# Kernel optimization log

Measured on AMD Instinct MI355X. Metric: run time of the kernel, lower is better.

The kernel has to match this reference:

```python
import jax, jax.numpy as jnp
import numpy as np

B, N, H, HID, LOCALITY = 2, 4096, 4, 256, 30.0
VD = HID // H
F32_MAX = jnp.finfo(jnp.float32).max


def setup_inputs() -> dict:
    key = jax.random.key(0)
    k1, k2, k3, k4 = jax.random.split(key, 4)
    m_dist = jax.random.uniform(k1, (B, N, N), dtype=jnp.float32)  # pairwise distances (b,N,N)
    x = jax.random.normal(k2, (B, N, HID), dtype=jnp.float32)
    r = jax.random.normal(k3, (1, H, 1, 1), dtype=jnp.float32)  # learned per-head distance scale
    # lecun_normal: std = 1/sqrt(fan_in), fan_in = HID
    weight = jax.random.normal(k4, (H, HID, VD), dtype=jnp.float32) / np.sqrt(HID)
    return {"m_dist": m_dist, "x": x, "r": r, "weight": weight}


def reference(m_dist, x, r, weight):
    # scaled distance per head: (b,h,n,n)
    scaled = m_dist[:, None, :, :] * (r ** 2)
    # percentile-thresholded local mask (linear interpolation, per row)
    thresh = jnp.percentile(scaled, LOCALITY, axis=-1, keepdims=True, method="linear")
    scaled = jnp.where(scaled <= thresh, scaled, F32_MAX)
    att = jax.nn.softmax(-scaled, axis=-1)  # (b,h,n,n)
    value = jnp.einsum("bnj,hjk->bhnk", x, weight)  # (b,h,n,v)
    out = jnp.einsum("bhnj,bhjd->bhnd", att, value)  # (b,h,n,v)
    out = jnp.transpose(out, (0, 2, 1, 3)).reshape(out.shape[0], -1, HID)  # (b,n,hid)
    return jax.nn.gelu(out, approximate=False)
```

## Files before the change

### kernel.cpp

```cpp
#include <hip/hip_runtime.h>
#include <hip/hip_bf16.h>

#define Bc   2
#define Nc   4096
#define Hc   4
#define HIDc 256
#define VDc  64

typedef short s8v  __attribute__((ext_vector_type(8)));
typedef float f4v  __attribute__((ext_vector_type(4)));

static __device__ __forceinline__ unsigned short bf16bits(float f) {
    __hip_bfloat16 h = __float2bfloat16(f);
    return *(unsigned short*)&h;
}

__global__ __launch_bounds__(256) void front_kernel(
    const float* __restrict__ m_dist, const float* __restrict__ wgt,
    unsigned short* __restrict__ wh, unsigned short* __restrict__ wl,
    float* __restrict__ thr_out, float* __restrict__ min_out)
{
    int t = threadIdx.x, bid = blockIdx.x;

    if (bid < 128) {
        int h  = bid >> 5;
        int kt = (bid >> 3) & 3;
        int jc = bid & 7;
        int lane = t >> 2, ii = t & 3;
        #pragma unroll
        for (int u = 0; u < 2; u++) {
            int i = ii * 2 + u;
            int j = jc * 32 + (lane >> 4) * 8 + i;
            int k = kt * 16 + (lane & 15);
            float v = wgt[((size_t)h * HIDc + j) * VDc + k];
            __hip_bfloat16 hb = __float2bfloat16(v);
            float hf = __bfloat162float(hb);
            size_t o = ((((size_t)h * 4 + kt) * 8 + jc) * 64 + lane) * 8 + i;
            wh[o] = *(unsigned short*)&hb;
            wl[o] = bf16bits(v - hf);
        }
        return;
    }

    __shared__ unsigned int hist[1024];
    __shared__ float wredf[4];
    __shared__ unsigned int wsum[4];
    __shared__ unsigned int wscan[4];
    __shared__ int b0s, b1s;
    __shared__ unsigned int c0s;
    __shared__ unsigned int ncand;
    __shared__ float cand[256];
    __shared__ float s0s, s1s;

    size_t rowid = bid - 128;
    const float* row = m_dist + rowid * Nc;

    float4 vals[4];
    float lmin = 1e30f;
    #pragma unroll
    for (int i = 0; i < 4; i++) {
        float4 v = ((const float4*)row)[t + i * 256];
        vals[i] = v;
        lmin = fminf(lmin, fminf(fminf(v.x, v.y), fminf(v.z, v.w)));
    }
    #pragma unroll
    for (int o = 32; o > 0; o >>= 1) lmin = fminf(lmin, __shfl_xor(lmin, o));
    if ((t & 63) == 0) wredf[t >> 6] = lmin;

    const unsigned int R0 = 1228u, R1 = 1229u;
    float wlo = 0.25f, whi = 0.35f;
    int b0 = 0, b1 = 0;
    unsigned int C0 = 0;

    for (;;) {
        float wscale = 1024.0f / (whi - wlo);

        for (int i = t; i < 1024; i += 256) hist[i] = 0u;
        if (t == 0) ncand = 0u;
        __syncthreads();

        unsigned int cb = 0;
        #pragma unroll
        for (int i = 0; i < 4; i++) {
            float a[4] = {vals[i].x, vals[i].y, vals[i].z, vals[i].w};
            #pragma unroll
            for (int j = 0; j < 4; j++) {
                float v = a[j];
                if (v < wlo) {
                    cb++;
                } else {
                    int bx = (int)((v - wlo) * wscale);
                    if (bx < 1024) atomicAdd(&hist[bx], 1u);
                }
            }
        }
        #pragma unroll
        for (int o = 32; o > 0; o >>= 1) cb += __shfl_xor(cb, o);
        if ((t & 63) == 0) wsum[t >> 6] = cb;
        __syncthreads();
        unsigned int Cb = wsum[0] + wsum[1] + wsum[2] + wsum[3];

        unsigned int c[4], csum = 0;
        #pragma unroll
        for (int j = 0; j < 4; j++) { c[j] = hist[t * 4 + j]; csum += c[j]; }
        unsigned int inc = csum;
        #pragma unroll
        for (int o = 1; o < 64; o <<= 1) {
            unsigned int nv = __shfl_up(inc, o);
            if ((t & 63) >= o) inc += nv;
        }
        if ((t & 63) == 63) wscan[t >> 6] = inc;
        __syncthreads();
        unsigned int wpref = 0;
        for (int wv = 0; wv < (t >> 6); wv++) wpref += wscan[wv];
        unsigned int T = wscan[0] + wscan[1] + wscan[2] + wscan[3];
        unsigned int P = Cb + wpref + inc - csum;

        unsigned int cum = P;
        #pragma unroll
        for (int j = 0; j < 4; j++) {
            unsigned int lo = cum, hi = cum + c[j];
            if (R0 >= lo && R0 < hi) { b0s = t * 4 + j; c0s = lo; }
            if (R1 >= lo && R1 < hi) { b1s = t * 4 + j; }
            cum = hi;
        }
        __syncthreads();

        if (Cb <= R0 && R1 < Cb + T) { b0 = b0s; b1 = b1s; C0 = c0s; break; }
        wlo = 0.0f; whi = 1.001f;
    }

    float wscale = 1024.0f / (whi - wlo);
    #pragma unroll
    for (int i = 0; i < 4; i++) {
        float a[4] = {vals[i].x, vals[i].y, vals[i].z, vals[i].w};
        #pragma unroll
        for (int j = 0; j < 4; j++) {
            float v = a[j];
            if (v >= wlo) {
                int bx = (int)((v - wlo) * wscale);
                if (bx >= b0 && bx <= b1) {
                    unsigned int p = atomicAdd(&ncand, 1u);
                    if (p < 256u) cand[p] = v;
                }
            }
        }
    }
    __syncthreads();
    unsigned int nc = min(ncand, 256u);
    if ((unsigned int)t < nc) {
        float v = cand[t];
        unsigned int rk = C0;
        for (unsigned int j = 0; j < nc; j++) {
            float u = cand[j];
            rk += (u < v || (u == v && j < (unsigned int)t)) ? 1u : 0u;
        }
        if (rk == R0) s0s = v;
        if (rk == R1) s1s = v;
    }
    __syncthreads();
    if (t == 0) {
        thr_out[rowid] = 0.5f * (s0s + s1s);
        min_out[rowid] = fminf(fminf(wredf[0], wredf[1]), fminf(wredf[2], wredf[3]));
    }
}

__global__ __launch_bounds__(256) void value_kernel(
    const float* __restrict__ x,
    const unsigned short* __restrict__ wh, const unsigned short* __restrict__ wl,
    unsigned short* __restrict__ vt_g)
{
    int t  = threadIdx.x;
    int bid = blockIdx.x;
    int nt = bid & 63;
    int h  = (bid >> 6) & 3;
    int b  = bid >> 8;
    int n0 = nt * 64;

    int w = t >> 6, lane = t & 63, q4 = lane >> 4, m16 = lane & 15;
    int nb = n0 + w * 16;

    const float* xp = x + ((size_t)(b * Nc + nb + m16)) * HIDc + q4 * 8;

    f4v acc[4];
    #pragma unroll
    for (int kt = 0; kt < 4; kt++) acc[kt] = (f4v){0.f, 0.f, 0.f, 0.f};

    #pragma unroll
    for (int jc = 0; jc < 8; jc++) {
        float4 xv0 = *(const float4*)(xp + jc * 32);
        float4 xv1 = *(const float4*)(xp + jc * 32 + 4);
        float f[8] = {xv0.x, xv0.y, xv0.z, xv0.w, xv1.x, xv1.y, xv1.z, xv1.w};
        union { s8v v; unsigned short u[8]; } hs, ls;
        #pragma unroll
        for (int i = 0; i < 8; i++) {
            __hip_bfloat16 hb = __float2bfloat16(f[i]);
            float hf = __bfloat162float(hb);
            hs.u[i] = *(unsigned short*)&hb;
            ls.u[i] = bf16bits(f[i] - hf);
        }
        #pragma unroll
        for (int kt = 0; kt < 4; kt++) {
            size_t ao = (((size_t)(h * 4 + kt) * 8 + jc) << 9) + lane * 8;
            s8v ah = *(const s8v*)(wh + ao);
            s8v al = *(const s8v*)(wl + ao);
            acc[kt] = __builtin_amdgcn_mfma_f32_16x16x32_bf16(ah, hs.v, acc[kt], 0, 0, 0);
            acc[kt] = __builtin_amdgcn_mfma_f32_16x16x32_bf16(al, hs.v, acc[kt], 0, 0, 0);
            acc[kt] = __builtin_amdgcn_mfma_f32_16x16x32_bf16(ah, ls.v, acc[kt], 0, 0, 0);
        }
    }

    unsigned short* vg = vt_g + (((size_t)b * Hc + h) * VDc) * Nc;
    #pragma unroll
    for (int kt = 0; kt < 4; kt++) {
        #pragma unroll
        for (int rg = 0; rg < 4; rg++) {
            int k = kt * 16 + q4 * 4 + rg;
            vg[(size_t)k * Nc + nb + m16] = bf16bits(acc[kt][rg]);
        }
    }
}

#define NT 64
#define JT 32

__global__ __launch_bounds__(1024, 8) void attn_kernel(
    const float* __restrict__ m_dist, const float* __restrict__ rr,
    const unsigned short* __restrict__ vt_g,
    const float* __restrict__ thr_g, const float* __restrict__ min_g,
    float* __restrict__ Op, float* __restrict__ Zp, int jlen)
{
    __shared__ unsigned short vt[2][Hc * VDc * JT];

    int t = threadIdx.x;
    const int nblk = Bc * (Nc / NT);
    int js = blockIdx.x / nblk;
    int rb = blockIdx.x - js * nblk;
    int b  = rb >> 6;
    int n0 = (rb & 63) * NT;
    int j0 = js * jlen;

    int lane = t & 63, q = lane >> 4, m16 = lane & 15;
    int w = t >> 6;
    int h = w & 3, rq = w >> 2;
    int row = rq * 16 + m16;

    float mn  = min_g[b * Nc + n0 + row];
    float thm = thr_g[b * Nc + n0 + row];
    float rv = rr[h];
    float cc = -(rv * rv) * 1.4426950408889634f;
    float nmncc = -mn * cc;

    f4v acc[4];
    #pragma unroll
    for (int ct = 0; ct < 4; ct++) acc[ct] = (f4v){0.f, 0.f, 0.f, 0.f};
    float zacc = 0.f;

    const float* arow = m_dist + ((size_t)b * Nc + n0 + row) * Nc + j0 + q * 8;

    const unsigned short* vtb = vt_g + ((size_t)b * Hc * VDc) * Nc + j0;
    int vrow = t >> 2;
    int vlc  = (t & 3) ^ (vrow & 3);
    const unsigned short* vsrc = vtb + (size_t)vrow * Nc + vlc * 8;

    int bco = (q ^ (m16 & 3)) << 3;

    int niter = jlen / JT;

    __builtin_amdgcn_global_load_lds(
        (const __attribute__((address_space(1))) void*)(vsrc),
        (__attribute__((address_space(3))) void*)(&vt[0][(size_t)t * 8]),
        16, 0, 0);

    int cur = 0;
    for (int it = 0; it < niter; ++it) {
        __syncthreads();

        if (it + 1 < niter) {
            int jn = (it + 1) * JT;
            __builtin_amdgcn_global_load_lds(
                (const __attribute__((address_space(1))) void*)(vsrc + jn),
                (__attribute__((address_space(3))) void*)(&vt[cur ^ 1][(size_t)t * 8]),
                16, 0, 0);
        }

        float4 a0 = *(const float4*)(arow + it * JT);
        float4 a1 = *(const float4*)(arow + it * JT + 4);
        const unsigned short* vb = &vt[cur][h * VDc * JT];
        float w0 = (a0.x <= thm) ? __builtin_amdgcn_exp2f(__builtin_fmaf(a0.x, cc, nmncc)) : 0.f;
        float w1 = (a0.y <= thm) ? __builtin_amdgcn_exp2f(__builtin_fmaf(a0.y, cc, nmncc)) : 0.f;
        float w2 = (a0.z <= thm) ? __builtin_amdgcn_exp2f(__builtin_fmaf(a0.z, cc, nmncc)) : 0.f;
        float w3 = (a0.w <= thm) ? __builtin_amdgcn_exp2f(__builtin_fmaf(a0.w, cc, nmncc)) : 0.f;
        float w4 = (a1.x <= thm) ? __builtin_amdgcn_exp2f(__builtin_fmaf(a1.x, cc, nmncc)) : 0.f;
        float w5 = (a1.y <= thm) ? __builtin_amdgcn_exp2f(__builtin_fmaf(a1.y, cc, nmncc)) : 0.f;
        float w6 = (a1.z <= thm) ? __builtin_amdgcn_exp2f(__builtin_fmaf(a1.z, cc, nmncc)) : 0.f;
        float w7 = (a1.w <= thm) ? __builtin_amdgcn_exp2f(__builtin_fmaf(a1.w, cc, nmncc)) : 0.f;
        zacc += ((w0 + w1) + (w2 + w3)) + ((w4 + w5) + (w6 + w7));
        union { s8v v; __hip_bfloat162 h2[4]; } afu;
        afu.h2[0] = __float22bfloat162_rn((float2){w0, w1});
        afu.h2[1] = __float22bfloat162_rn((float2){w2, w3});
        afu.h2[2] = __float22bfloat162_rn((float2){w4, w5});
        afu.h2[3] = __float22bfloat162_rn((float2){w6, w7});
        #pragma unroll
        for (int ct = 0; ct < 4; ct++) {
            int brow = ct * 16 + m16;
            s8v bf = *(const s8v*)(vb + brow * JT + bco);
            acc[ct] = __builtin_amdgcn_mfma_f32_16x16x32_bf16(afu.v, bf, acc[ct], 0, 0, 0);
        }
        cur ^= 1;
    }

    zacc += __shfl_xor(zacc, 16);
    zacc += __shfl_xor(zacc, 32);
    if (q == 0)
        Zp[(((size_t)js * Bc + b) * Hc + h) * Nc + n0 + row] = zacc;

    #pragma unroll
    for (int ct = 0; ct < 4; ct++) {
        #pragma unroll
        for (int rg = 0; rg < 4; rg++) {
            int nl = rq * 16 + q * 4 + rg;
            Op[(((size_t)js * Bc + b) * Nc + n0 + nl) * HIDc + h * VDc + ct * 16 + m16]
                = acc[ct][rg];
        }
    }
}

__global__ __launch_bounds__(256) void combine_kernel(
    const float* __restrict__ Op, const float* __restrict__ Zp,
    float* __restrict__ out, int S)
{
    int g = blockIdx.x * 256 + threadIdx.x;
    int c4 = g & 63;
    int n  = (g >> 6) & (Nc - 1);
    int b  = g >> 18;
    int h  = c4 >> 4;

    float z = 0.f;
    float4 v = {0.f, 0.f, 0.f, 0.f};
    for (int s = 0; s < S; s++) {
        z += Zp[(((size_t)s * Bc + b) * Hc + h) * Nc + n];
        float4 p = *(const float4*)&Op[(((size_t)s * Bc + b) * Nc + n) * HIDc + c4 * 4];
        v.x += p.x; v.y += p.y; v.z += p.z; v.w += p.w;
    }
    float iz = 1.0f / z;
    float4 o;
    float u;
    u = v.x * iz; o.x = 0.5f * u * (1.0f + erff(u * 0.7071067811865476f));
    u = v.y * iz; o.y = 0.5f * u * (1.0f + erff(u * 0.7071067811865476f));
    u = v.z * iz; o.z = 0.5f * u * (1.0f + erff(u * 0.7071067811865476f));
    u = v.w * iz; o.w = 0.5f * u * (1.0f + erff(u * 0.7071067811865476f));
    *(float4*)&out[(((size_t)b * Nc + n) * HIDc) + c4 * 4] = o;
}

extern "C" void kernel_launch(void* const* d_in, const int* in_sizes, int n_in,
                              void* d_out, int out_size, void* d_ws, size_t ws_size,
                              hipStream_t stream) {
    const float* m_dist = (const float*)d_in[0];
    const float* x      = (const float*)d_in[1];
    const float* r      = (const float*)d_in[2];
    const float* weight = (const float*)d_in[3];
    float* out = (float*)d_out;

    char* ws = (char*)d_ws;
    const size_t MB = 1024 * 1024;
    unsigned short* vt = (unsigned short*)ws;
    float* thr = (float*)(ws + 4 * MB);
    float* mn  = (float*)(ws + 4 * MB + 32 * 1024);
    float* Zp  = (float*)(ws + 4 * MB + 64 * 1024);
    float* Op  = (float*)(ws + 5 * MB);

    const size_t OpSz = (size_t)Bc * Nc * HIDc * 4;
    int S = 4;
    if (ws_size < 6 * MB + 4 * OpSz) S = 2;
    if (ws_size < 6 * MB + 2 * OpSz) S = 1;
    int jlen = Nc / S;

    char* pb = ws + 5 * MB + (size_t)S * OpSz;
    unsigned short* wh = (unsigned short*)pb;
    unsigned short* wl = (unsigned short*)(pb + 128 * 1024);

    front_kernel<<<128 + Bc * Nc, 256, 0, stream>>>(m_dist, weight, wh, wl, thr, mn);
    value_kernel<<<512, 256, 0, stream>>>(x, wh, wl, vt);
    attn_kernel<<<S * Bc * (Nc / NT), 1024, 0, stream>>>(m_dist, r, vt, thr, mn, Op, Zp, jlen);
    combine_kernel<<<(Bc * Nc * HIDc) / 1024, 256, 0, stream>>>(Op, Zp, out, S);
}
```

Baseline: 293.9 us.

## Double j-tile width and software-prefetch distance rows one tile ahead

Widens the j tile from 32 to 64 columns, so each iteration issues two MFMA groups and the LDS value tile is staged with two async global-to-LDS loads per thread, using a wider 8-way XOR swizzle. The first half of each row's m_dist data is prefetched into registers one iteration ahead. This halves the number of barriers per row block and hides global load latency. In exchange it doubles LDS use per block and raises register pressure under the 1024-thread, 8-wave launch bound.

```diff
diff --git a/kernel.cpp b/kernel.cpp
--- a/kernel.cpp
+++ b/kernel.cpp
@@ -222,7 +222,7 @@
 }
 
 #define NT 64
-#define JT 32
+#define JT 64
 
 __global__ __launch_bounds__(1024, 8) void attn_kernel(
     const float* __restrict__ m_dist, const float* __restrict__ rr,
@@ -259,56 +259,96 @@
     const float* arow = m_dist + ((size_t)b * Nc + n0 + row) * Nc + j0 + q * 8;
 
     const unsigned short* vtb = vt_g + ((size_t)b * Hc * VDc) * Nc + j0;
-    int vrow = t >> 2;
-    int vlc  = (t & 3) ^ (vrow & 3);
-    const unsigned short* vsrc = vtb + (size_t)vrow * Nc + vlc * 8;
-
-    int bco = (q ^ (m16 & 3)) << 3;
+    const unsigned short* vsrc  = vtb + (size_t)(t >> 3) * Nc + (((t & 7) ^ ((t >> 3) & 7)) << 3);
+    const unsigned short* vsrc2 = vsrc + (size_t)128 * Nc;
+
+    int bc0 = ((q ^ (m16 & 7)) << 3);
+    int bc1 = (((4 + q) ^ (m16 & 7)) << 3);
+    const int hoff = h * VDc * JT;
 
     int niter = jlen / JT;
 
-    __builtin_amdgcn_global_load_lds(
-        (const __attribute__((address_space(1))) void*)(vsrc),
-        (__attribute__((address_space(3))) void*)(&vt[0][(size_t)t * 8]),
-        16, 0, 0);
+    #define STAGE(k, bi) do {                                                    \
+        size_t jo_ = (size_t)(k) * JT;                                           \
+        __builtin_amdgcn_global_load_lds(                                        \
+            (const __attribute__((address_space(1))) void*)(vsrc + jo_),         \
+            (__attribute__((address_space(3))) void*)                            \
+                ((char*)&vt[bi][0] + (size_t)t * 16),                            \
+            16, 0, 0);                                                           \
+        __builtin_amdgcn_global_load_lds(                                        \
+            (const __attribute__((address_space(1))) void*)(vsrc2 + jo_),        \
+            (__attribute__((address_space(3))) void*)                            \
+                ((char*)&vt[bi][0] + 16384 + (size_t)t * 16),                    \
+            16, 0, 0);                                                           \
+    } while (0)
+
+    STAGE(0, 0);
+    float4 pf0 = *(const float4*)(arow);
+    float4 pf1 = *(const float4*)(arow + 4);
 
     int cur = 0;
     for (int it = 0; it < niter; ++it) {
         __syncthreads();
 
+        int jt = it * JT;
+        float4 c0 = pf0, c1 = pf1;
+        float4 c2 = *(const float4*)(arow + jt + 32);
+        float4 c3 = *(const float4*)(arow + jt + 36);
         if (it + 1 < niter) {
-            int jn = (it + 1) * JT;
-            __builtin_amdgcn_global_load_lds(
-                (const __attribute__((address_space(1))) void*)(vsrc + jn),
-                (__attribute__((address_space(3))) void*)(&vt[cur ^ 1][(size_t)t * 8]),
-                16, 0, 0);
-        }
-
-        float4 a0 = *(const float4*)(arow + it * JT);
-        float4 a1 = *(const float4*)(arow + it * JT + 4);
-        const unsigned short* vb = &vt[cur][h * VDc * JT];
-        float w0 = (a0.x <= thm) ? __builtin_amdgcn_exp2f(__builtin_fmaf(a0.x, cc, nmncc)) : 0.f;
-        float w1 = (a0.y <= thm) ? __builtin_amdgcn_exp2f(__builtin_fmaf(a0.y, cc, nmncc)) : 0.f;
-        float w2 = (a0.z <= thm) ? __builtin_amdgcn_exp2f(__builtin_fmaf(a0.z, cc, nmncc)) : 0.f;
-        float w3 = (a0.w <= thm) ? __builtin_amdgcn_exp2f(__builtin_fmaf(a0.w, cc, nmncc)) : 0.f;
-        float w4 = (a1.x <= thm) ? __builtin_amdgcn_exp2f(__builtin_fmaf(a1.x, cc, nmncc)) : 0.f;
-        float w5 = (a1.y <= thm) ? __builtin_amdgcn_exp2f(__builtin_fmaf(a1.y, cc, nmncc)) : 0.f;
-        float w6 = (a1.z <= thm) ? __builtin_amdgcn_exp2f(__builtin_fmaf(a1.z, cc, nmncc)) : 0.f;
-        float w7 = (a1.w <= thm) ? __builtin_amdgcn_exp2f(__builtin_fmaf(a1.w, cc, nmncc)) : 0.f;
-        zacc += ((w0 + w1) + (w2 + w3)) + ((w4 + w5) + (w6 + w7));
-        union { s8v v; __hip_bfloat162 h2[4]; } afu;
-        afu.h2[0] = __float22bfloat162_rn((float2){w0, w1});
-        afu.h2[1] = __float22bfloat162_rn((float2){w2, w3});
-        afu.h2[2] = __float22bfloat162_rn((float2){w4, w5});
-        afu.h2[3] = __float22bfloat162_rn((float2){w6, w7});
-        #pragma unroll
-        for (int ct = 0; ct < 4; ct++) {
-            int brow = ct * 16 + m16;
-            s8v bf = *(const s8v*)(vb + brow * JT + bco);
-            acc[ct] = __builtin_amdgcn_mfma_f32_16x16x32_bf16(afu.v, bf, acc[ct], 0, 0, 0);
+            pf0 = *(const float4*)(arow + jt + 64);
+            pf1 = *(const float4*)(arow + jt + 68);
+            STAGE(it + 1, cur ^ 1);
+        }
+
+        const unsigned short* vb = &vt[cur][hoff];
+
+        {
+            float w0 = (c0.x <= thm) ? __builtin_amdgcn_exp2f(__builtin_fmaf(c0.x, cc, nmncc)) : 0.f;
+            float w1 = (c0.y <= thm) ? __builtin_amdgcn_exp2f(__builtin_fmaf(c0.y, cc, nmncc)) : 0.f;
+            float w2 = (c0.z <= thm) ? __builtin_amdgcn_exp2f(__builtin_fmaf(c0.z, cc, nmncc)) : 0.f;
+            float w3 = (c0.w <= thm) ? __builtin_amdgcn_exp2f(__builtin_fmaf(c0.w, cc, nmncc)) : 0.f;
+            float w4 = (c1.x <= thm) ? __builtin_amdgcn_exp2f(__builtin_fmaf(c1.x, cc, nmncc)) : 0.f;
+            float w5 = (c1.y <= thm) ? __builtin_amdgcn_exp2f(__builtin_fmaf(c1.y, cc, nmncc)) : 0.f;
+            float w6 = (c1.z <= thm) ? __builtin_amdgcn_exp2f(__builtin_fmaf(c1.z, cc, nmncc)) : 0.f;
+            float w7 = (c1.w <= thm) ? __builtin_amdgcn_exp2f(__builtin_fmaf(c1.w, cc, nmncc)) : 0.f;
+            zacc += ((w0 + w1) + (w2 + w3)) + ((w4 + w5) + (w6 + w7));
+            union { s8v v; __hip_bfloat162 h2[4]; } afu;
+            afu.h2[0] = __float22bfloat162_rn((float2){w0, w1});
+            afu.h2[1] = __float22bfloat162_rn((float2){w2, w3});
+            afu.h2[2] = __float22bfloat162_rn((float2){w4, w5});
+            afu.h2[3] = __float22bfloat162_rn((float2){w6, w7});
+            #pragma unroll
+            for (int ct = 0; ct < 4; ct++) {
+                int brow = ct * 16 + m16;
+                s8v bf = *(const s8v*)(vb + brow * JT + bc0);
+                acc[ct] = __builtin_amdgcn_mfma_f32_16x16x32_bf16(afu.v, bf, acc[ct], 0, 0, 0);
+            }
+        }
+        {
+            float w0 = (c2.x <= thm) ? __builtin_amdgcn_exp2f(__builtin_fmaf(c2.x, cc, nmncc)) : 0.f;
+            float w1 = (c2.y <= thm) ? __builtin_amdgcn_exp2f(__builtin_fmaf(c2.y, cc, nmncc)) : 0.f;
+            float w2 = (c2.z <= thm) ? __builtin_amdgcn_exp2f(__builtin_fmaf(c2.z, cc, nmncc)) : 0.f;
+            float w3 = (c2.w <= thm) ? __builtin_amdgcn_exp2f(__builtin_fmaf(c2.w, cc, nmncc)) : 0.f;
+            float w4 = (c3.x <= thm) ? __builtin_amdgcn_exp2f(__builtin_fmaf(c3.x, cc, nmncc)) : 0.f;
+            float w5 = (c3.y <= thm) ? __builtin_amdgcn_exp2f(__builtin_fmaf(c3.y, cc, nmncc)) : 0.f;
+            float w6 = (c3.z <= thm) ? __builtin_amdgcn_exp2f(__builtin_fmaf(c3.z, cc, nmncc)) : 0.f;
+            float w7 = (c3.w <= thm) ? __builtin_amdgcn_exp2f(__builtin_fmaf(c3.w, cc, nmncc)) : 0.f;
+            zacc += ((w0 + w1) + (w2 + w3)) + ((w4 + w5) + (w6 + w7));
+            union { s8v v; __hip_bfloat162 h2[4]; } afu;
+            afu.h2[0] = __float22bfloat162_rn((float2){w0, w1});
+            afu.h2[1] = __float22bfloat162_rn((float2){w2, w3});
+            afu.h2[2] = __float22bfloat162_rn((float2){w4, w5});
+            afu.h2[3] = __float22bfloat162_rn((float2){w6, w7});
+            #pragma unroll
+            for (int ct = 0; ct < 4; ct++) {
+                int brow = ct * 16 + m16;
+                s8v bf = *(const s8v*)(vb + brow * JT + bc1);
+                acc[ct] = __builtin_amdgcn_mfma_f32_16x16x32_bf16(afu.v, bf, acc[ct], 0, 0, 0);
+            }
         }
         cur ^= 1;
     }
+    #undef STAGE
 
     zacc += __shfl_xor(zacc, 16);
     zacc += __shfl_xor(zacc, 32);
```

After: 415.0 us. 1.41x slower.
